# Kernel tuning notes

Measured on AMD Instinct MI355X. Metric: run time of the kernel, lower is better.

## Reference

```python
import jax, jax.numpy as jnp
import numpy as np
import math

B, S, D, H = 2, 2048, 1024, 16
DK = D // H


def setup_inputs() -> dict:
    key = jax.random.key(0)
    ks = jax.random.split(key, 12)
    scale = 1.0 / math.sqrt(D)
    inp = {
        "query": jax.random.normal(ks[0], (B, S, D), jnp.float32),
        "key": jax.random.normal(ks[1], (B, S, D), jnp.float32),
        "value": jax.random.normal(ks[2], (B, S, D), jnp.float32),
        # causal 0/1 mask, broadcast over heads
        "mask": jnp.broadcast_to(jnp.tril(jnp.ones((S, S), jnp.int32)), (B, 1, S, S)),
        "Wq": jax.random.normal(ks[3], (D, D), jnp.float32) * scale,
        "bq": jnp.zeros((D,), jnp.float32),
        "Wk": jax.random.normal(ks[4], (D, D), jnp.float32) * scale,
        "bk": jnp.zeros((D,), jnp.float32),
        "Wv": jax.random.normal(ks[5], (D, D), jnp.float32) * scale,
        "bv": jnp.zeros((D,), jnp.float32),
        "Wo": jax.random.normal(ks[6], (D, D), jnp.float32) * scale,
        "bo": jnp.zeros((D,), jnp.float32),
    }
    return inp


def _split_heads(x):
    # [B,S,D] -> [B,H,S,DK]
    return x.reshape(B, S, H, DK).transpose(0, 2, 1, 3)


def reference(query, key, value, mask, Wq, bq, Wk, bk, Wv, bv, Wo, bo):
    q = _split_heads(query @ Wq.T + bq)
    k = _split_heads(key @ Wk.T + bk)
    v = _split_heads(value @ Wv.T + bv)
    # scaled dot-product attention with additive mask (mask==0 -> -inf)
    scores = jnp.einsum("bhqd,bhkd->bhqk", q, k) / math.sqrt(DK)
    scores = jnp.where(mask == 0, -jnp.inf, scores)
    w = jax.nn.softmax(scores, axis=-1)
    out = jnp.einsum("bhqk,bhkd->bhqd", w, v)
    out = out.transpose(0, 2, 1, 3).reshape(B, S, D)
    return out @ Wo.T + bo
```

## Files before the change

kernel.cpp:

```cpp
#include <hip/hip_runtime.h>
#include <hip/hip_bf16.h>
#include <math.h>

#define BBATCH 2
#define SSEQ 2048
#define DMODEL 1024
#define NH 16
#define MTOT (BBATCH*SSEQ)

typedef short bfrag __attribute__((ext_vector_type(8)));
typedef float ffrag __attribute__((ext_vector_type(4)));
typedef float f16frag __attribute__((ext_vector_type(16)));
typedef unsigned int uiv2 __attribute__((ext_vector_type(2)));

typedef const __attribute__((address_space(1))) unsigned int* gas_t;
typedef __attribute__((address_space(3))) unsigned int* las_t;

__device__ __forceinline__ void dl16(const void* g, void* l) {
  __builtin_amdgcn_global_load_lds((gas_t)(unsigned long long)g,
                                   (las_t)(unsigned int)(unsigned long long)l,
                                   16, 0, 0);
}

__device__ __forceinline__ void drain_vm() {
  asm volatile("s_waitcnt vmcnt(0)" ::: "memory");
}

#if defined(__has_builtin) && __has_builtin(__builtin_amdgcn_exp2f)
__device__ __forceinline__ float fexp2(float x) { return __builtin_amdgcn_exp2f(x); }
#else
__device__ __forceinline__ float fexp2(float x) { return exp2f(x); }
#endif

#if defined(__has_builtin) && __has_builtin(__builtin_amdgcn_permlane32_swap)
__device__ __forceinline__ void pl32swap(unsigned &a, unsigned &b) {
  uiv2 r = __builtin_amdgcn_permlane32_swap(a, b, false, false);
  a = r[0]; b = r[1];
}
#else
__device__ __forceinline__ void pl32swap(unsigned &a, unsigned &b) {
  asm volatile("v_permlane32_swap_b32 %0, %1" : "+v"(a), "+v"(b));
}
#endif

__device__ __forceinline__ unsigned short f2bf(float f) {
  union { float f; unsigned u; } v; v.f = f;
  unsigned r = v.u + 0x7fffu + ((v.u >> 16) & 1u);
  return (unsigned short)(r >> 16);
}

__device__ __forceinline__ unsigned pkbf2(float a, float b) {
  float2 f; f.x = a; f.y = b;
  union { __hip_bfloat162 h; unsigned u; } cv;
  cv.h = __float22bfloat162_rn(f);
  return cv.u;
}

__global__ __launch_bounds__(256) void convert_all_kernel(
    const float* __restrict__ q, const float* __restrict__ k, const float* __restrict__ v,
    const float* __restrict__ wq, const float* __restrict__ wk,
    const float* __restrict__ wv, const float* __restrict__ wo,
    unsigned short* __restrict__ dst)
{
  const long NIN = (long)MTOT * DMODEL;
  const long NW  = (long)DMODEL * DMODEL;
  const long total8 = (3 * NIN + 4 * NW) >> 3;
  long i8 = (long)blockIdx.x * blockDim.x + threadIdx.x;
  const long stride = (long)gridDim.x * blockDim.x;
  for (; i8 < total8; i8 += stride) {
    const long i = i8 << 3;
    const float* src; long off;
    if (i < NIN)          { src = q; off = i; }
    else if (i < 2 * NIN) { src = k; off = i - NIN; }
    else if (i < 3 * NIN) { src = v; off = i - 2 * NIN; }
    else {
      const long j = i - 3 * NIN;
      const int wsel = (int)(j >> 20);
      off = j & (NW - 1);
      src = (wsel == 0) ? wq : (wsel == 1) ? wk : (wsel == 2) ? wv : wo;
    }
    const float4 x0 = *(const float4*)(src + off);
    const float4 x1 = *(const float4*)(src + off + 4);
    ushort4 o0, o1;
    o0.x = f2bf(x0.x); o0.y = f2bf(x0.y); o0.z = f2bf(x0.z); o0.w = f2bf(x0.w);
    o1.x = f2bf(x1.x); o1.y = f2bf(x1.y); o1.z = f2bf(x1.z); o1.w = f2bf(x1.w);
    union { ushort4 s[2]; uint4 u; } pk; pk.s[0] = o0; pk.s[1] = o1;
    *(uint4*)(dst + i) = pk.u;
  }
}

struct ProjArgs {
  const unsigned short* X[3];
  const unsigned short* W[3];
  const float* bias[3];
  unsigned short* dst[3];
  float scale[3];
};

__global__ __launch_bounds__(256, 2) void qkv_proj(ProjArgs a)
{
  __shared__ alignas(16) unsigned short As[2][128 * 64];
  __shared__ alignas(16) unsigned short Bs[2][128 * 64];
  const int t = threadIdx.x;
  const int lane = t & 63, w = t >> 6;
  const int quad = lane >> 4, l16 = lane & 15;
  const int m0 = blockIdx.x * 128;
  const int n0 = blockIdx.y * 128;
  const int z = blockIdx.z;
  const unsigned short* __restrict__ X = a.X[z];
  const unsigned short* __restrict__ W = a.W[z];
  const int wm = (w & 1) * 64, wn = (w >> 1) * 64;

  int sw[2];
#pragma unroll
  for (int c = 0; c < 2; ++c) sw[c] = (((c * 4 + quad) ^ (l16 & 7)) * 8);

  ffrag acc[4][4];
#pragma unroll
  for (int i = 0; i < 4; ++i)
#pragma unroll
    for (int j = 0; j < 4; ++j)
#pragma unroll
      for (int e = 0; e < 4; ++e) acc[i][j][e] = 0.f;

#pragma unroll
  for (int i = 0; i < 4; ++i) {
    const int ch = i * 256 + t;
    const int row = ch >> 3, lc = (ch & 7) ^ (row & 7);
    dl16(X + (size_t)(m0 + row) * DMODEL + lc * 8, As[0] + ch * 8);
    dl16(W + (size_t)(n0 + row) * DMODEL + lc * 8, Bs[0] + ch * 8);
  }

  for (int kk = 0; kk < 16; ++kk) {
    const int cur = kk & 1;
    drain_vm();
    __syncthreads();

    if (kk < 15) {
      const int k1 = (kk + 1) * 64, nxt = cur ^ 1;
#pragma unroll
      for (int i = 0; i < 4; ++i) {
        const int ch = i * 256 + t;
        const int row = ch >> 3, lc = (ch & 7) ^ (row & 7);
        dl16(X + (size_t)(m0 + row) * DMODEL + k1 + lc * 8, As[nxt] + ch * 8);
        dl16(W + (size_t)(n0 + row) * DMODEL + k1 + lc * 8, Bs[nxt] + ch * 8);
      }
    }

    bfrag af[4][2], bg[4][2];
#pragma unroll
    for (int fi = 0; fi < 4; ++fi)
#pragma unroll
      for (int c = 0; c < 2; ++c) {
        af[fi][c] = *(const bfrag*)&As[cur][(wm + fi * 16 + l16) * 64 + sw[c]];
        bg[fi][c] = *(const bfrag*)&Bs[cur][(wn + fi * 16 + l16) * 64 + sw[c]];
      }
#pragma unroll
    for (int c = 0; c < 2; ++c)
#pragma unroll
      for (int fi = 0; fi < 4; ++fi)
#pragma unroll
        for (int fj = 0; fj < 4; ++fj)
          acc[fi][fj] = __builtin_amdgcn_mfma_f32_16x16x32_bf16(af[fi][c], bg[fj][c], acc[fi][fj], 0, 0, 0);
  }

  const float sc = a.scale[z];
  const float* __restrict__ bias = a.bias[z];
  unsigned short* __restrict__ dst = a.dst[z];
#pragma unroll
  for (int fj = 0; fj < 4; ++fj) {
    const int n = n0 + wn + fj * 16 + l16;
    const float bv = bias[n];
    const int h = n >> 6, dk = n & 63;
    if (z < 2) {
#pragma unroll
      for (int fi = 0; fi < 4; ++fi)
#pragma unroll
        for (int r = 0; r < 4; ++r) {
          const int m = m0 + wm + fi * 16 + quad * 4 + r;
          const int b_ = m >> 11, s_ = m & (SSEQ - 1);
          dst[((size_t)(b_ * NH + h) * SSEQ + s_) * 64 + dk] = f2bf((acc[fi][fj][r] + bv) * sc);
        }
    } else {
#pragma unroll
      for (int fi = 0; fi < 4; ++fi) {
        const int m = m0 + wm + fi * 16 + quad * 4;
        const int b_ = m >> 11, s_ = m & (SSEQ - 1);
        const int jt = s_ >> 6, kl = s_ & 63;
        ushort4 pk;
        pk.x = f2bf(acc[fi][fj][0] + bv);
        pk.y = f2bf(acc[fi][fj][1] + bv);
        pk.z = f2bf(acc[fi][fj][2] + bv);
        pk.w = f2bf(acc[fi][fj][3] + bv);
        *(ushort4*)&dst[(((size_t)(b_ * NH + h) * 32 + jt) * 64 + dk) * 64 + kl] = pk;
      }
    }
  }
}

__global__ __launch_bounds__(256, 2) void out_proj(
    const unsigned short* __restrict__ X,
    const unsigned short* __restrict__ W,
    const float* __restrict__ bias,
    float* __restrict__ Y)
{
  __shared__ alignas(16) unsigned short As[2][128 * 64];
  __shared__ alignas(16) unsigned short Bs[2][64 * 64];
  const int t = threadIdx.x;
  const int lane = t & 63, w = t >> 6;
  const int quad = lane >> 4, l16 = lane & 15;
  const int m0 = blockIdx.x * 128;
  const int n0 = blockIdx.y * 64;
  const int wm = (w & 1) * 64, wn = (w >> 1) * 32;

  int sw[2];
#pragma unroll
  for (int c = 0; c < 2; ++c) sw[c] = (((c * 4 + quad) ^ (l16 & 7)) * 8);

  ffrag acc[4][2];
#pragma unroll
  for (int i = 0; i < 4; ++i)
#pragma unroll
    for (int j = 0; j < 2; ++j)
#pragma unroll
      for (int e = 0; e < 4; ++e) acc[i][j][e] = 0.f;

#pragma unroll
  for (int i = 0; i < 4; ++i) {
    const int ch = i * 256 + t;
    const int row = ch >> 3, lc = (ch & 7) ^ (row & 7);
    dl16(X + (size_t)(m0 + row) * DMODEL + lc * 8, As[0] + ch * 8);
  }
#pragma unroll
  for (int i = 0; i < 2; ++i) {
    const int ch = i * 256 + t;
    const int row = ch >> 3, lc = (ch & 7) ^ (row & 7);
    dl16(W + (size_t)(n0 + row) * DMODEL + lc * 8, Bs[0] + ch * 8);
  }

  for (int kk = 0; kk < 16; ++kk) {
    const int cur = kk & 1;
    drain_vm();
    __syncthreads();

    if (kk < 15) {
      const int k1 = (kk + 1) * 64, nxt = cur ^ 1;
#pragma unroll
      for (int i = 0; i < 4; ++i) {
        const int ch = i * 256 + t;
        const int row = ch >> 3, lc = (ch & 7) ^ (row & 7);
        dl16(X + (size_t)(m0 + row) * DMODEL + k1 + lc * 8, As[nxt] + ch * 8);
      }
#pragma unroll
      for (int i = 0; i < 2; ++i) {
        const int ch = i * 256 + t;
        const int row = ch >> 3, lc = (ch & 7) ^ (row & 7);
        dl16(W + (size_t)(n0 + row) * DMODEL + k1 + lc * 8, Bs[nxt] + ch * 8);
      }
    }

    bfrag af[4][2], bg[2][2];
#pragma unroll
    for (int fi = 0; fi < 4; ++fi)
#pragma unroll
      for (int c = 0; c < 2; ++c)
        af[fi][c] = *(const bfrag*)&As[cur][(wm + fi * 16 + l16) * 64 + sw[c]];
#pragma unroll
    for (int fj = 0; fj < 2; ++fj)
#pragma unroll
      for (int c = 0; c < 2; ++c)
        bg[fj][c] = *(const bfrag*)&Bs[cur][(wn + fj * 16 + l16) * 64 + sw[c]];
#pragma unroll
    for (int c = 0; c < 2; ++c)
#pragma unroll
      for (int fi = 0; fi < 4; ++fi)
#pragma unroll
        for (int fj = 0; fj < 2; ++fj)
          acc[fi][fj] = __builtin_amdgcn_mfma_f32_16x16x32_bf16(af[fi][c], bg[fj][c], acc[fi][fj], 0, 0, 0);
  }

#pragma unroll
  for (int fj = 0; fj < 2; ++fj) {
    const int n = n0 + wn + fj * 16 + l16;
    const float bv = bias[n];
#pragma unroll
    for (int fi = 0; fi < 4; ++fi)
#pragma unroll
      for (int r = 0; r < 4; ++r) {
        const int m = m0 + wm + fi * 16 + quad * 4 + r;
        Y[(size_t)m * DMODEL + n] = acc[fi][fj][r] + bv;
      }
  }
}

__global__ __launch_bounds__(256, 4) void attn_mfma(
    const unsigned short* __restrict__ Q,
    const unsigned short* __restrict__ K,
    const unsigned short* __restrict__ Vt_g,
    unsigned short* __restrict__ ctx)
{
  __shared__ alignas(16) unsigned short Kb[2][64 * 64];
  __shared__ alignas(16) unsigned short Vb[2][64 * 64];

  const int t = threadIdx.x;
  const int lane = t & 63, w = t >> 6;
  const int l31 = lane & 31, h = lane >> 5;
  const int bid = blockIdx.x;
  const int xcd = bid & 7;
  const int j_  = bid >> 3;
  const int bh = xcd * 4 + (j_ >> 4);
  const int x  = j_ & 15;
  const int qt_lo = x, qt_hi = 31 - x;
  const int qsel = w >> 1;
  const int qt_w = qsel ? qt_hi : qt_lo;
  const int i0_w = qt_w * 64;
  const int q0 = (w & 1) * 32;
  const int qloc = q0 + l31;
  const int b_ = bh >> 4, h_ = bh & (NH - 1);

  const unsigned short* kg = K + (size_t)bh * SSEQ * 64;
  const unsigned short* vg = Vt_g + (size_t)bh * SSEQ * 64;

  int koff[2], loff[2];
#pragma unroll
  for (int i = 0; i < 2; ++i) {
    const int ch = i * 256 + t;
    const int r = ch >> 3;
    const int lc = (ch & 7) ^ (r & 7);
    koff[i] = r * 64 + lc * 8;
    loff[i] = ch * 8;
  }
  int pc[4];
#pragma unroll
  for (int ks = 0; ks < 4; ++ks) pc[ks] = ((ks * 2 + h) ^ (l31 & 7)) * 8;
  const int rb0 = l31 * 64, rb1 = (32 + l31) * 64;

#pragma unroll
  for (int i = 0; i < 2; ++i) {
    dl16(kg + koff[i], Kb[0] + loff[i]);
    dl16(vg + koff[i], Vb[0] + loff[i]);
  }

  const unsigned short* qrow = Q + ((size_t)bh * SSEQ + i0_w + qloc) * 64;
  bfrag qb[4];
#pragma unroll
  for (int ks = 0; ks < 4; ++ks)
    qb[ks] = *(const bfrag*)(qrow + ks * 16 + h * 8);

  f16frag o0, o1;
#pragma unroll
  for (int e = 0; e < 16; ++e) { o0[e] = 0.f; o1[e] = 0.f; }
  float lacc = 0.f;

  for (int jt = 0; jt <= qt_hi; ++jt) {
    const int cur = jt & 1;
    drain_vm();
    __syncthreads();

    if (jt < qt_hi) {
      const int nxt = cur ^ 1;
      const size_t tb = (size_t)(jt + 1) * 4096;
#pragma unroll
      for (int i = 0; i < 2; ++i) {
        dl16(kg + tb + koff[i], Kb[nxt] + loff[i]);
        dl16(vg + tb + koff[i], Vb[nxt] + loff[i]);
      }
    }

    if (jt <= qt_w) {
      f16frag s0, s1;
#pragma unroll
      for (int e = 0; e < 16; ++e) { s0[e] = 0.f; s1[e] = 0.f; }
#pragma unroll
      for (int ks = 0; ks < 4; ++ks) {
        bfrag ka0 = *(const bfrag*)&Kb[cur][rb0 + pc[ks]];
        bfrag ka1 = *(const bfrag*)&Kb[cur][rb1 + pc[ks]];
        s0 = __builtin_amdgcn_mfma_f32_32x32x16_bf16(ka0, qb[ks], s0, 0, 0, 0);
        s1 = __builtin_amdgcn_mfma_f32_32x32x16_bf16(ka1, qb[ks], s1, 0, 0, 0);
      }

      const bool diag = (jt == qt_w);
      float p0[16], p1[16];
#pragma unroll
      for (int r = 0; r < 16; ++r) { p0[r] = fexp2(s0[r]); p1[r] = fexp2(s1[r]); }
      if (diag) {
#pragma unroll
        for (int r = 0; r < 16; ++r) {
          const int keyl = (r & 3) + 8 * (r >> 2) + 4 * h;
          if (keyl > qloc)      p0[r] = 0.f;
          if (keyl + 32 > qloc) p1[r] = 0.f;
        }
      }
      float ss = 0.f;
#pragma unroll
      for (int r = 0; r < 16; r += 4)
        ss += ((p0[r] + p0[r + 1]) + (p0[r + 2] + p0[r + 3])) +
              ((p1[r] + p1[r + 1]) + (p1[r + 2] + p1[r + 3]));
      lacc += ss;

      bfrag pb[4];
#pragma unroll
      for (int ks = 0; ks < 4; ++ks) {
        const float* pp = (ks >> 1) ? p1 : p0;
        const int kb = (ks & 1) * 8;
        unsigned w0 = pkbf2(pp[kb + 0], pp[kb + 1]);
        unsigned w1 = pkbf2(pp[kb + 2], pp[kb + 3]);
        unsigned w2 = pkbf2(pp[kb + 4], pp[kb + 5]);
        unsigned w3 = pkbf2(pp[kb + 6], pp[kb + 7]);
        pl32swap(w0, w2);
        pl32swap(w1, w3);
        union { unsigned u[4]; bfrag f; } cv;
        cv.u[0] = w0; cv.u[1] = w1; cv.u[2] = w2; cv.u[3] = w3;
        pb[ks] = cv.f;
      }

#pragma unroll
      for (int ks = 0; ks < 4; ++ks) {
        bfrag va0 = *(const bfrag*)&Vb[cur][rb0 + pc[ks]];
        bfrag va1 = *(const bfrag*)&Vb[cur][rb1 + pc[ks]];
        o0 = __builtin_amdgcn_mfma_f32_32x32x16_bf16(va0, pb[ks], o0, 0, 0, 0);
        o1 = __builtin_amdgcn_mfma_f32_32x32x16_bf16(va1, pb[ks], o1, 0, 0, 0);
      }
    }
  }

  const float lfull = lacc + __shfl_xor(lacc, 32, 64);
  const float inv = 1.f / lfull;
  unsigned short* cb = ctx + (size_t)(b_ * SSEQ + i0_w + qloc) * DMODEL + h_ * 64;
#pragma unroll
  for (int g = 0; g < 4; ++g) {
    const int dkb = 8 * g + 4 * h;
    union { __hip_bfloat162 hh[2]; unsigned long long u; } cv;
    float2 lo, hi;
    lo.x = o0[4 * g + 0] * inv; lo.y = o0[4 * g + 1] * inv;
    hi.x = o0[4 * g + 2] * inv; hi.y = o0[4 * g + 3] * inv;
    cv.hh[0] = __float22bfloat162_rn(lo);
    cv.hh[1] = __float22bfloat162_rn(hi);
    *(unsigned long long*)(cb + dkb) = cv.u;
    lo.x = o1[4 * g + 0] * inv; lo.y = o1[4 * g + 1] * inv;
    hi.x = o1[4 * g + 2] * inv; hi.y = o1[4 * g + 3] * inv;
    cv.hh[0] = __float22bfloat162_rn(lo);
    cv.hh[1] = __float22bfloat162_rn(hi);
    *(unsigned long long*)(cb + 32 + dkb) = cv.u;
  }
}

extern "C" void kernel_launch(void* const* d_in, const int* in_sizes, int n_in,
                              void* d_out, int out_size, void* d_ws, size_t ws_size,
                              hipStream_t stream)
{
  const float* q  = (const float*)d_in[0];
  const float* k  = (const float*)d_in[1];
  const float* v  = (const float*)d_in[2];
  const float* wq = (const float*)d_in[4];
  const float* bq = (const float*)d_in[5];
  const float* wk = (const float*)d_in[6];
  const float* bk = (const float*)d_in[7];
  const float* wv = (const float*)d_in[8];
  const float* bv = (const float*)d_in[9];
  const float* wo = (const float*)d_in[10];
  const float* bo = (const float*)d_in[11];

  const long NIN = (long)MTOT * DMODEL;
  const long NW  = (long)DMODEL * DMODEL;
  unsigned short* ws16 = (unsigned short*)d_ws;
  unsigned short* qx  = ws16;
  unsigned short* kx  = qx + NIN;
  unsigned short* vx  = kx + NIN;
  unsigned short* wqb = vx + NIN;
  unsigned short* wkb = wqb + NW;
  unsigned short* wvb = wkb + NW;
  unsigned short* wob = wvb + NW;
  unsigned short* Qp  = wob + NW;
  unsigned short* Kp  = Qp + NIN;
  unsigned short* Vp  = Kp + NIN;
  unsigned short* Cx  = Vp + NIN;

  convert_all_kernel<<<2048, 256, 0, stream>>>(q, k, v, wq, wk, wv, wo, ws16);

  ProjArgs pa;
  pa.X[0] = qx;  pa.X[1] = kx;  pa.X[2] = vx;
  pa.W[0] = wqb; pa.W[1] = wkb; pa.W[2] = wvb;
  pa.bias[0] = bq; pa.bias[1] = bk; pa.bias[2] = bv;
  pa.dst[0] = Qp; pa.dst[1] = Kp; pa.dst[2] = Vp;
  pa.scale[0] = 0.18033688011112042f;
  pa.scale[1] = 1.0f;
  pa.scale[2] = 1.0f;
  qkv_proj<<<dim3(MTOT / 128, DMODEL / 128, 3), 256, 0, stream>>>(pa);

  attn_mfma<<<512, 256, 0, stream>>>(Qp, Kp, Vp, Cx);

  out_proj<<<dim3(MTOT / 128, DMODEL / 64), 256, 0, stream>>>(Cx, wob, bo, (float*)d_out);
}
```

Before: 221.3 us.

## Split attention key tiles across two wave groups and reduce partials via LDS

The attention kernel now launches 512 threads per block. Waves are split by key-tile parity, so each pair of key tiles is loaded per stage and processed in parallel by two wave groups. Partial outputs and row sums are then combined through shared memory before normalization and store. This halves the serial key-loop length per wave and doubles the waves in flight. In exchange it uses more LDS (32KB plus reduction reuse), adds an extra reduction barrier, and may lower occupancy with launch_bounds(512,4).

```diff
diff --git a/kernel.cpp b/kernel.cpp
--- a/kernel.cpp
+++ b/kernel.cpp
@@ -293,14 +293,14 @@
   }
 }
 
-__global__ __launch_bounds__(256, 4) void attn_mfma(
+__global__ __launch_bounds__(512, 4) void attn_mfma(
     const unsigned short* __restrict__ Q,
     const unsigned short* __restrict__ K,
     const unsigned short* __restrict__ Vt_g,
     unsigned short* __restrict__ ctx)
 {
-  __shared__ alignas(16) unsigned short Kb[2][64 * 64];
-  __shared__ alignas(16) unsigned short Vb[2][64 * 64];
+  __shared__ alignas(16) unsigned short Kb[2][2][64 * 64];
+  __shared__ alignas(16) unsigned short Vb[2][2][64 * 64];
 
   const int t = threadIdx.x;
   const int lane = t & 63, w = t >> 6;
@@ -311,34 +311,32 @@
   const int bh = xcd * 4 + (j_ >> 4);
   const int x  = j_ & 15;
   const int qt_lo = x, qt_hi = 31 - x;
-  const int qsel = w >> 1;
+  const int qsel = w >> 2;
+  const int par  = (w >> 1) & 1;
   const int qt_w = qsel ? qt_hi : qt_lo;
   const int i0_w = qt_w * 64;
   const int q0 = (w & 1) * 32;
   const int qloc = q0 + l31;
   const int b_ = bh >> 4, h_ = bh & (NH - 1);
+  const int NTs = (qt_hi >> 1) + 1;
 
   const unsigned short* kg = K + (size_t)bh * SSEQ * 64;
   const unsigned short* vg = Vt_g + (size_t)bh * SSEQ * 64;
 
-  int koff[2], loff[2];
-#pragma unroll
-  for (int i = 0; i < 2; ++i) {
-    const int ch = i * 256 + t;
-    const int r = ch >> 3;
-    const int lc = (ch & 7) ^ (r & 7);
-    koff[i] = r * 64 + lc * 8;
-    loff[i] = ch * 8;
-  }
+  const int r = t >> 3;
+  const int lc = (t & 7) ^ (r & 7);
+  const int goff = r * 64 + lc * 8;
+  const int loff = t * 8;
+
   int pc[4];
 #pragma unroll
   for (int ks = 0; ks < 4; ++ks) pc[ks] = ((ks * 2 + h) ^ (l31 & 7)) * 8;
   const int rb0 = l31 * 64, rb1 = (32 + l31) * 64;
 
 #pragma unroll
-  for (int i = 0; i < 2; ++i) {
-    dl16(kg + koff[i], Kb[0] + loff[i]);
-    dl16(vg + koff[i], Vb[0] + loff[i]);
+  for (int p = 0; p < 2; ++p) {
+    dl16(kg + p * 4096 + goff, Kb[0][p] + loff);
+    dl16(vg + p * 4096 + goff, Vb[0][p] + loff);
   }
 
   const unsigned short* qrow = Q + ((size_t)bh * SSEQ + i0_w + qloc) * 64;
@@ -352,29 +350,30 @@
   for (int e = 0; e < 16; ++e) { o0[e] = 0.f; o1[e] = 0.f; }
   float lacc = 0.f;
 
-  for (int jt = 0; jt <= qt_hi; ++jt) {
-    const int cur = jt & 1;
+  for (int st = 0; st < NTs; ++st) {
+    const int cur = st & 1;
     drain_vm();
     __syncthreads();
 
-    if (jt < qt_hi) {
+    if (st + 1 < NTs) {
       const int nxt = cur ^ 1;
-      const size_t tb = (size_t)(jt + 1) * 4096;
-#pragma unroll
-      for (int i = 0; i < 2; ++i) {
-        dl16(kg + tb + koff[i], Kb[nxt] + loff[i]);
-        dl16(vg + tb + koff[i], Vb[nxt] + loff[i]);
-      }
-    }
-
+      const size_t base = (size_t)(st + 1) * 8192;
+#pragma unroll
+      for (int p = 0; p < 2; ++p) {
+        dl16(kg + base + p * 4096 + goff, Kb[nxt][p] + loff);
+        dl16(vg + base + p * 4096 + goff, Vb[nxt][p] + loff);
+      }
+    }
+
+    const int jt = st * 2 + par;
     if (jt <= qt_w) {
       f16frag s0, s1;
 #pragma unroll
       for (int e = 0; e < 16; ++e) { s0[e] = 0.f; s1[e] = 0.f; }
 #pragma unroll
       for (int ks = 0; ks < 4; ++ks) {
-        bfrag ka0 = *(const bfrag*)&Kb[cur][rb0 + pc[ks]];
-        bfrag ka1 = *(const bfrag*)&Kb[cur][rb1 + pc[ks]];
+        bfrag ka0 = *(const bfrag*)&Kb[cur][par][rb0 + pc[ks]];
+        bfrag ka1 = *(const bfrag*)&Kb[cur][par][rb1 + pc[ks]];
         s0 = __builtin_amdgcn_mfma_f32_32x32x16_bf16(ka0, qb[ks], s0, 0, 0, 0);
         s1 = __builtin_amdgcn_mfma_f32_32x32x16_bf16(ka1, qb[ks], s1, 0, 0, 0);
       }
@@ -382,20 +381,20 @@
       const bool diag = (jt == qt_w);
       float p0[16], p1[16];
 #pragma unroll
-      for (int r = 0; r < 16; ++r) { p0[r] = fexp2(s0[r]); p1[r] = fexp2(s1[r]); }
+      for (int rr = 0; rr < 16; ++rr) { p0[rr] = fexp2(s0[rr]); p1[rr] = fexp2(s1[rr]); }
       if (diag) {
 #pragma unroll
-        for (int r = 0; r < 16; ++r) {
-          const int keyl = (r & 3) + 8 * (r >> 2) + 4 * h;
-          if (keyl > qloc)      p0[r] = 0.f;
-          if (keyl + 32 > qloc) p1[r] = 0.f;
+        for (int rr = 0; rr < 16; ++rr) {
+          const int keyl = (rr & 3) + 8 * (rr >> 2) + 4 * h;
+          if (keyl > qloc)      p0[rr] = 0.f;
+          if (keyl + 32 > qloc) p1[rr] = 0.f;
         }
       }
       float ss = 0.f;
 #pragma unroll
-      for (int r = 0; r < 16; r += 4)
-        ss += ((p0[r] + p0[r + 1]) + (p0[r + 2] + p0[r + 3])) +
-              ((p1[r] + p1[r + 1]) + (p1[r + 2] + p1[r + 3]));
+      for (int rr = 0; rr < 16; rr += 4)
+        ss += ((p0[rr] + p0[rr + 1]) + (p0[rr + 2] + p0[rr + 3])) +
+              ((p1[rr] + p1[rr + 1]) + (p1[rr + 2] + p1[rr + 3]));
       lacc += ss;
 
       bfrag pb[4];
@@ -416,32 +415,54 @@
 
 #pragma unroll
       for (int ks = 0; ks < 4; ++ks) {
-        bfrag va0 = *(const bfrag*)&Vb[cur][rb0 + pc[ks]];
-        bfrag va1 = *(const bfrag*)&Vb[cur][rb1 + pc[ks]];
+        bfrag va0 = *(const bfrag*)&Vb[cur][par][rb0 + pc[ks]];
+        bfrag va1 = *(const bfrag*)&Vb[cur][par][rb1 + pc[ks]];
         o0 = __builtin_amdgcn_mfma_f32_32x32x16_bf16(va0, pb[ks], o0, 0, 0, 0);
         o1 = __builtin_amdgcn_mfma_f32_32x32x16_bf16(va1, pb[ks], o1, 0, 0, 0);
       }
     }
   }
 
-  const float lfull = lacc + __shfl_xor(lacc, 32, 64);
-  const float inv = 1.f / lfull;
-  unsigned short* cb = ctx + (size_t)(b_ * SSEQ + i0_w + qloc) * DMODEL + h_ * 64;
-#pragma unroll
-  for (int g = 0; g < 4; ++g) {
-    const int dkb = 8 * g + 4 * h;
-    union { __hip_bfloat162 hh[2]; unsigned long long u; } cv;
-    float2 lo, hi;
-    lo.x = o0[4 * g + 0] * inv; lo.y = o0[4 * g + 1] * inv;
-    hi.x = o0[4 * g + 2] * inv; hi.y = o0[4 * g + 3] * inv;
-    cv.hh[0] = __float22bfloat162_rn(lo);
-    cv.hh[1] = __float22bfloat162_rn(hi);
-    *(unsigned long long*)(cb + dkb) = cv.u;
-    lo.x = o1[4 * g + 0] * inv; lo.y = o1[4 * g + 1] * inv;
-    hi.x = o1[4 * g + 2] * inv; hi.y = o1[4 * g + 3] * inv;
-    cv.hh[0] = __float22bfloat162_rn(lo);
-    cv.hh[1] = __float22bfloat162_rn(hi);
-    *(unsigned long long*)(cb + 32 + dkb) = cv.u;
+  __syncthreads();
+  const int mw = qsel * 2 + (w & 1);
+  float* ob = (float*)&Kb[0][0][0] + mw * 2048;
+  float* lb = (float*)&Vb[0][0][0] + mw * 64;
+  if (par == 1) {
+#pragma unroll
+    for (int e = 0; e < 16; ++e) {
+      ob[e * 64 + lane]        = o0[e];
+      ob[(16 + e) * 64 + lane] = o1[e];
+    }
+    lb[lane] = lacc;
+  }
+  __syncthreads();
+  if (par == 0) {
+#pragma unroll
+    for (int e = 0; e < 16; ++e) {
+      o0[e] += ob[e * 64 + lane];
+      o1[e] += ob[(16 + e) * 64 + lane];
+    }
+    lacc += lb[lane];
+
+    const float lfull = lacc + __shfl_xor(lacc, 32, 64);
+    const float inv = 1.f / lfull;
+    unsigned short* cb = ctx + (size_t)(b_ * SSEQ + i0_w + qloc) * DMODEL + h_ * 64;
+#pragma unroll
+    for (int g = 0; g < 4; ++g) {
+      const int dkb = 8 * g + 4 * h;
+      union { __hip_bfloat162 hh[2]; unsigned long long u; } cv;
+      float2 lo, hi;
+      lo.x = o0[4 * g + 0] * inv; lo.y = o0[4 * g + 1] * inv;
+      hi.x = o0[4 * g + 2] * inv; hi.y = o0[4 * g + 3] * inv;
+      cv.hh[0] = __float22bfloat162_rn(lo);
+      cv.hh[1] = __float22bfloat162_rn(hi);
+      *(unsigned long long*)(cb + dkb) = cv.u;
+      lo.x = o1[4 * g + 0] * inv; lo.y = o1[4 * g + 1] * inv;
+      hi.x = o1[4 * g + 2] * inv; hi.y = o1[4 * g + 3] * inv;
+      cv.hh[0] = __float22bfloat162_rn(lo);
+      cv.hh[1] = __float22bfloat162_rn(hi);
+      *(unsigned long long*)(cb + 32 + dkb) = cv.u;
+    }
   }
 }
 
@@ -488,7 +509,7 @@
   pa.scale[2] = 1.0f;
   qkv_proj<<<dim3(MTOT / 128, DMODEL / 128, 3), 256, 0, stream>>>(pa);
 
-  attn_mfma<<<512, 256, 0, stream>>>(Qp, Kp, Vp, Cx);
+  attn_mfma<<<512, 512, 0, stream>>>(Qp, Kp, Vp, Cx);
 
   out_proj<<<dim3(MTOT / 128, DMODEL / 64), 256, 0, stream>>>(Cx, wob, bo, (float*)d_out);
 }
```

New measurement: 212.5 us (median of 2 runs). -4.0%, faster.
